# Optimization experiments

Measured on AMD Instinct MI355X. Metric: run time of the kernel, lower is better.

Reference implementation:

```python
import jax, jax.numpy as jnp
import numpy as np
from functools import partial

N_NODES = 50000
N_EDGES = 600000
N_FEAT = 128
HID = [128, 64, 32, 16]
N_GRAPHS = 64
N_CLASSES = 10


def gcn_conv(x, W, b, src, dst, n_nodes):
    # PyG GCNConv: h = x @ W; propagate with symmetric norm over A + I; add bias.
    h = x @ W  # [N, out]
    ones = jnp.ones((src.shape[0],), dtype=x.dtype)
    deg = jax.ops.segment_sum(ones, dst, num_segments=n_nodes) + 1.0  # self-loop
    dinv = jax.lax.rsqrt(deg)
    coef = dinv[src] * dinv[dst]  # [E]
    agg = jax.ops.segment_sum(h[src] * coef[:, None], dst, num_segments=n_nodes)
    agg = agg + h * (dinv * dinv)[:, None]  # self-loop contribution
    return agg + b


def global_mean_pool(x, batch, n_graphs):
    s = jax.ops.segment_sum(x, batch, num_segments=n_graphs)
    cnt = jax.ops.segment_sum(jnp.ones((x.shape[0],), x.dtype), batch, num_segments=n_graphs)
    return s / jnp.maximum(cnt, 1.0)[:, None]


def setup_inputs() -> dict:
    key = jax.random.key(0)
    ks = jax.random.split(key, 16)
    x = jax.random.normal(ks[0], (N_NODES, N_FEAT), dtype=jnp.float32)
    edge_index = jax.random.randint(ks[1], (2, N_EDGES), 0, N_NODES, dtype=jnp.int64)
    batch = jnp.sort(jax.random.randint(ks[2], (N_NODES,), 0, N_GRAPHS, dtype=jnp.int64))

    def glorot(k, fan_in, fan_out):
        s = float(np.sqrt(6.0 / (fan_in + fan_out)))
        return jax.random.uniform(k, (fan_in, fan_out), jnp.float32, -s, s)

    dims = [N_FEAT] + HID
    params = {}
    for i in range(4):
        params[f"W{i+1}"] = glorot(ks[3 + i], dims[i], dims[i + 1])
        params[f"b{i+1}"] = jnp.zeros((dims[i + 1],), jnp.float32)
    params["Wlin"] = glorot(ks[7], HID[-1], N_CLASSES)
    params["blin"] = jnp.zeros((N_CLASSES,), jnp.float32)
    return {"x": x, "edge_index": edge_index, "batch": batch, **params}


def reference(x, edge_index, batch, W1, b1, W2, b2, W3, b3, W4, b4, Wlin, blin):
    src, dst = edge_index[0], edge_index[1]
    n = x.shape[0]
    h = jax.nn.relu(gcn_conv(x, W1, b1, src, dst, n))
    h = jax.nn.relu(gcn_conv(h, W2, b2, src, dst, n))
    h = jax.nn.relu(gcn_conv(h, W3, b3, src, dst, n))
    h = jax.nn.relu(gcn_conv(h, W4, b4, src, dst, n))
    g = global_mean_pool(h, batch, N_GRAPHS)  # [G, 16]
    return g @ Wlin + blin
```

## Files before the change

### kernel.cpp

```cpp
#include <hip/hip_runtime.h>
#include <hip/hip_bf16.h>


#define N_GRAPHS 64
#define N_CLASSES 10

typedef short bf8_t __attribute__((ext_vector_type(8)));
typedef float f4_t  __attribute__((ext_vector_type(4)));

__device__ __forceinline__ float b2f(unsigned int u) {
  return __uint_as_float(u << 16);
}
__device__ __forceinline__ unsigned short f2b(float f) {
  unsigned int x = __float_as_uint(f);
  x += 0x7fffu + ((x >> 16) & 1u);
  return (unsigned short)(x >> 16);
}

__device__ __forceinline__ void block_detect(const unsigned int* __restrict__ xraw,
    const unsigned int* __restrict__ eraw, int* f32, int* i64) {
  __shared__ int c_bf, c_nz;
  if (threadIdx.x == 0) { c_bf = 0; c_nz = 0; }
  __syncthreads();
  unsigned int d = xraw[threadIdx.x & 255];
  int e = (int)(((d & 0xffffu) >> 7) & 0xff);
  if (e >= 100 && e <= 140) atomicAdd(&c_bf, 1);
  if (eraw && threadIdx.x < 64 && eraw[2 * threadIdx.x + 1] != 0u) atomicAdd(&c_nz, 1);
  __syncthreads();
  *f32 = (c_bf < 150) ? 1 : 0;
  if (i64) *i64 = (c_nz == 0) ? 1 : 0;
}

struct WPtrs { const void* p[10]; };
static constexpr int WSEG[10] = {16384, 128, 8192, 64, 2048, 32, 512, 16, 160, 10};
static constexpr int WTOTAL   = 27546;
static constexpr int WOFF[10] = {0, 16384, 16512, 24704, 24768, 26816, 26848, 27360, 27376, 27536};

__global__ __launch_bounds__(256) void cvtwe_gemm1_kernel(
    const unsigned int* __restrict__ xraw, WPtrs wp, unsigned short* __restrict__ wc,
    const int* __restrict__ braw, int* __restrict__ b32,
    const int* __restrict__ eraw, int* __restrict__ deg, int* __restrict__ rank,
    unsigned short* __restrict__ H,
    int G1, int BW, int BB, int n, int E) {
  __shared__ unsigned short Wlds2[2048];
  int f32, i64;
  block_detect(xraw, (const unsigned int*)eraw, &f32, &i64);
  const int bid = blockIdx.x;
  if (bid < G1) {
    const void* w1 = wp.p[0];
    const int l = threadIdx.x & 63;
    const int r16 = l & 15, quad = l >> 4;
    const int m0 = (bid * 4 + (threadIdx.x >> 6)) * 32;
    bf8_t afrag[2][4];
    #pragma unroll
    for (int mt = 0; mt < 2; ++mt) {
      int node = m0 + mt * 16 + r16;
      int nc = node < n ? node : n - 1;
      if (f32) {
        const float* xp = (const float*)xraw + (size_t)nc * 128 + quad * 8;
        #pragma unroll
        for (int kb = 0; kb < 4; ++kb) {
          const float4* p4 = (const float4*)(xp + kb * 32);
          float4 u0 = p4[0], u1 = p4[1];
          bf8_t a;
          a[0] = (short)f2b(u0.x); a[1] = (short)f2b(u0.y);
          a[2] = (short)f2b(u0.z); a[3] = (short)f2b(u0.w);
          a[4] = (short)f2b(u1.x); a[5] = (short)f2b(u1.y);
          a[6] = (short)f2b(u1.z); a[7] = (short)f2b(u1.w);
          afrag[mt][kb] = a;
        }
      } else {
        const unsigned short* xp = (const unsigned short*)xraw + (size_t)nc * 128 + quad * 8;
        #pragma unroll
        for (int kb = 0; kb < 4; ++kb)
          afrag[mt][kb] = *(const bf8_t*)(xp + kb * 32);
      }
    }
    for (int ct = 0; ct < 8; ++ct) {
      __syncthreads();
      #pragma unroll
      for (int it2 = 0; it2 < 2; ++it2) {
        int seg = it2 * 64 + (threadIdx.x >> 2);
        int c4  = threadIdx.x & 3;
        int kb = seg >> 5, quadk = (seg >> 3) & 3, j = seg & 7;
        int nnb = ct * 16 + c4 * 4;
        unsigned short w4[4];
        if (f32) {
          float4 u = *(const float4*)((const float*)w1 + seg * 128 + nnb);
          w4[0] = f2b(u.x); w4[1] = f2b(u.y); w4[2] = f2b(u.z); w4[3] = f2b(u.w);
        } else {
          ushort4 u = *(const ushort4*)((const unsigned short*)w1 + seg * 128 + nnb);
          w4[0] = u.x; w4[1] = u.y; w4[2] = u.z; w4[3] = u.w;
        }
        #pragma unroll
        for (int q4 = 0; q4 < 4; ++q4)
          Wlds2[kb * 512 + (quadk * 16 + c4 * 4 + q4) * 8 + j] = w4[q4];
      }
      __syncthreads();
      bf8_t bfrag[4];
      #pragma unroll
      for (int kb = 0; kb < 4; ++kb)
        bfrag[kb] = *(const bf8_t*)&Wlds2[kb * 512 + l * 8];
      #pragma unroll
      for (int mt = 0; mt < 2; ++mt) {
        f4_t acc = {0.f, 0.f, 0.f, 0.f};
        #pragma unroll
        for (int kb = 0; kb < 4; ++kb)
          acc = __builtin_amdgcn_mfma_f32_16x16x32_bf16(afrag[mt][kb], bfrag[kb], acc, 0, 0, 0);
        #pragma unroll
        for (int r = 0; r < 4; ++r) {
          int node = m0 + mt * 16 + quad * 4 + r;
          if (node < n)
            H[(size_t)node * 128 + ct * 16 + r16] = f2b(acc[r]);
        }
      }
    }
  } else if (bid < G1 + BW) {
    int i = (bid - G1) * 256 + threadIdx.x;
    if (i >= WTOTAL) return;
    int off = i, s = 0;
    #pragma unroll
    for (int t = 0; t < 10; ++t) {
      if (s == 0 && off >= WSEG[t]) { off -= WSEG[t]; } else if (s == 0) { s = t + 1; }
    }
    s -= 1;
    int soff = off;
    if ((s & 1) == 0 && s <= 6) {
      int KB, FOUT;
      if (s == 0)      { KB = 4; FOUT = 128; }
      else if (s == 2) { KB = 4; FOUT = 64; }
      else if (s == 4) { KB = 2; FOUT = 32; }
      else             { KB = 1; FOUT = 16; }
      int j = off & 7, l = (off >> 3) & 63, f = off >> 9;
      int ct = f / KB, kb = f - ct * KB;
      int k = kb * 32 + ((l >> 4) << 3) + j;
      int nn = ct * 16 + (l & 15);
      soff = k * FOUT + nn;
    }
    const void* p = wp.p[s];
    wc[WOFF[s] + off] = f32 ? f2b(((const float*)p)[soff])
                            : ((const unsigned short*)p)[soff];
  } else if (bid < G1 + BW + BB) {
    int i = (bid - G1 - BW) * 256 + threadIdx.x;
    if (i < n) b32[i] = i64 ? braw[2 * i] : braw[i];
  } else {
    int c = bid - G1 - BW - BB;
    #pragma unroll
    for (int r = 0; r < 2; ++r) {
      int e = c * 512 + r * 256 + threadIdx.x;
      if (e < E) {
        int d = i64 ? eraw[2 * (E + e)] : eraw[E + e];
        rank[e] = atomicAdd(&deg[d], 1);
      }
    }
  }
}

__global__ __launch_bounds__(256) void scan_kernel(const int* __restrict__ deg,
    int* __restrict__ row_ptr, float* __restrict__ dinv,
    unsigned long long* __restrict__ desc, uint2* __restrict__ csr, int n) {
  __shared__ int ws[4];
  __shared__ int s_total;
  __shared__ unsigned int s_prev;
  const int b = blockIdx.x, tid = threadIdx.x, lane = tid & 63, wv = tid >> 6;
  const int i = b * 256 + tid;
  int v = (i < n) ? (deg[i] + 1) : 0;
  int x = v;
  #pragma unroll
  for (int off = 1; off < 64; off <<= 1) {
    int y = __shfl_up(x, off, 64);
    if (lane >= off) x += y;
  }
  if (lane == 63) ws[wv] = x;
  __syncthreads();
  int wbase = 0;
  for (int w = 0; w < wv; ++w) wbase += ws[w];
  int incl = x + wbase;
  if (tid == 0) {
    int tot = ws[0] + ws[1] + ws[2] + ws[3];
    s_total = tot;
    unsigned long long st = (b == 0) ? (2ULL << 62) : (1ULL << 62);
    atomicExch(&desc[b], st | (unsigned long long)(unsigned int)tot);
    if (b == 0) s_prev = 0u;
  }
  __syncthreads();
  if (b > 0 && wv == 0) {
    unsigned int running = 0;
    int j = b - 1;
    while (true) {
      int idx = j - lane;
      unsigned long long d;
      if (idx >= 0) {
        do { d = atomicAdd(&desc[idx], 0ULL); } while ((d >> 62) == 0ULL);
      } else {
        d = (2ULL << 62);
      }
      unsigned long long ball = __ballot((d >> 62) == 2ULL);
      int fp = ball ? (__ffsll((unsigned long long)ball) - 1) : 64;
      unsigned int contrib = (lane <= fp) ? (unsigned int)(d & 0xffffffffULL) : 0u;
      #pragma unroll
      for (int o = 32; o; o >>= 1) contrib += __shfl_xor(contrib, o, 64);
      running += contrib;
      if (fp < 64) break;
      j -= 64;
    }
    if (lane == 0) {
      atomicExch(&desc[b], (2ULL << 62) |
                 (unsigned long long)(unsigned int)(running + (unsigned int)s_total));
      s_prev = running;
    }
  }
  __syncthreads();
  int tot = (int)s_prev + incl;
  if (i < n) {
    row_ptr[i + 1] = tot;
    float di = rsqrtf((float)v);
    dinv[i] = di;
    uint2 se;
    se.x = (unsigned int)i;
    se.y = __float_as_uint(di * di);
    csr[tot - v] = se;
  }
  if (i == 0) row_ptr[0] = 0;
}

__global__ __launch_bounds__(256) void fill_kernel(
    const int* __restrict__ eraw, const unsigned int* __restrict__ xraw,
    const int* __restrict__ row_ptr, const int* __restrict__ rank,
    const float* __restrict__ dinv, uint2* __restrict__ csr, int E) {
  int f32, i64;
  block_detect(xraw, (const unsigned int*)eraw, &f32, &i64);
  int e = blockIdx.x * 256 + threadIdx.x;
  if (e >= E) return;
  int s, d;
  if (i64) { s = eraw[2 * e]; d = eraw[2 * (E + e)]; }
  else     { s = eraw[e];     d = eraw[E + e]; }
  int pos = row_ptr[d] + 1 + rank[e];
  uint2 v;
  v.x = (unsigned int)s;
  v.y = __float_as_uint(dinv[s] * dinv[d]);
  csr[pos] = v;
}

__global__ __launch_bounds__(256) void aggemm1_mfma_kernel(
    const unsigned short* __restrict__ Hin,
    const int* __restrict__ row_ptr, const uint2* __restrict__ csr,
    const unsigned short* __restrict__ bias,
    const unsigned short* __restrict__ Wf,
    unsigned short* __restrict__ Hout, int n) {
  __shared__ __align__(16) unsigned short Gf[8 * 544];
  __shared__ __align__(16) unsigned short T[16 * 136];
  __shared__ int rp[17];
  __shared__ unsigned long long owner8[4];
  __shared__ __align__(16) unsigned short coefh[32];
  unsigned char* owner = (unsigned char*)owner8;
  const int tid = threadIdx.x;
  const int l = tid & 63, w = tid >> 6, l15 = l & 15, quad = l >> 4;
  const int node0 = blockIdx.x * 16;
  if (tid < 17) { int g = node0 + tid; rp[tid] = row_ptr[g < n ? g : n]; }
  __syncthreads();
  const int e0 = rp[0], e1 = rp[16];
  f4_t acc0 = {0.f, 0.f, 0.f, 0.f}, acc1 = {0.f, 0.f, 0.f, 0.f};
  const int s_slot = tid >> 3, qf = tid & 7;
  for (int sb = e0; sb < e1; sb += 32) {
    int gslot = sb + s_slot;
    bool valid = gslot < e1;
    uint2 ent = csr[valid ? gslot : e0];
    if (qf == 0) {
      float coef = valid ? __uint_as_float(ent.y) : 0.f;
      int m = 0;
      if (rp[m + 8] <= gslot) m += 8;
      if (rp[m + 4] <= gslot) m += 4;
      if (rp[m + 2] <= gslot) m += 2;
      if (rp[m + 1] <= gslot) m += 1;
      owner[s_slot] = (unsigned char)m;
      coefh[s_slot] = f2b(coef);
    }
    const unsigned int* hp = (const unsigned int*)Hin + (size_t)ent.x * 64 + qf * 8;
    uint4 v0 = *(const uint4*)hp;
    uint4 v1 = *(const uint4*)(hp + 4);
    unsigned int dws[8] = {v0.x, v0.y, v0.z, v0.w, v1.x, v1.y, v1.z, v1.w};
    unsigned short* gb = &Gf[qf * 544 + (s_slot >> 3) * 136 + (s_slot & 7)];
    #pragma unroll
    for (int d2 = 0; d2 < 8; ++d2) {
      gb[(d2 * 2) * 8]     = (unsigned short)(dws[d2] & 0xffffu);
      gb[(d2 * 2 + 1) * 8] = (unsigned short)(dws[d2] >> 16);
    }
    __syncthreads();
    unsigned long long ob = owner8[quad];
    bf8_t cf = *(const bf8_t*)&coefh[quad * 8];
    bf8_t af;
    #pragma unroll
    for (int j = 0; j < 8; ++j) {
      int o = (int)((ob >> (8 * j)) & 0xffULL);
      af[j] = (o == l15) ? cf[j] : (short)0;
    }
    {
      const int ct = w * 2;
      bf8_t bf0 = *(const bf8_t*)&Gf[ct * 544 + quad * 136 + l15 * 8];
      acc0 = __builtin_amdgcn_mfma_f32_16x16x32_bf16(af, bf0, acc0, 0, 0, 0);
      bf8_t bf1 = *(const bf8_t*)&Gf[(ct + 1) * 544 + quad * 136 + l15 * 8];
      acc1 = __builtin_amdgcn_mfma_f32_16x16x32_bf16(af, bf1, acc1, 0, 0, 0);
    }
    __syncthreads();
  }
  {
    const int ct = w * 2;
    float bv0 = b2f(bias[ct * 16 + l15]);
    float bv1 = b2f(bias[(ct + 1) * 16 + l15]);
    #pragma unroll
    for (int rr = 0; rr < 4; ++rr) {
      T[(quad * 4 + rr) * 136 + ct * 16 + l15]       = f2b(fmaxf(acc0[rr] + bv0, 0.f));
      T[(quad * 4 + rr) * 136 + (ct + 1) * 16 + l15] = f2b(fmaxf(acc1[rr] + bv1, 0.f));
    }
  }
  __syncthreads();
  f4_t a2 = {0.f, 0.f, 0.f, 0.f};
  #pragma unroll
  for (int kb = 0; kb < 4; ++kb) {
    bf8_t afr = *(const bf8_t*)&T[l15 * 136 + kb * 32 + quad * 8];
    bf8_t bfr = *(const bf8_t*)&Wf[((w * 4 + kb) * 64 + l) * 8];
    a2 = __builtin_amdgcn_mfma_f32_16x16x32_bf16(afr, bfr, a2, 0, 0, 0);
  }
  #pragma unroll
  for (int rr = 0; rr < 4; ++rr) {
    int node = node0 + quad * 4 + rr;
    if (node < n)
      Hout[(size_t)node * 64 + w * 16 + l15] = f2b(a2[rr]);
  }
}

template<int DW> struct UVec { unsigned int d[DW]; };
template<int DW>
__device__ __forceinline__ UVec<DW> uload(const unsigned int* p) {
  UVec<DW> r;
  if constexpr (DW == 4) { uint4 v = *(const uint4*)p; r.d[0]=v.x; r.d[1]=v.y; r.d[2]=v.z; r.d[3]=v.w; }
  else if constexpr (DW == 2) { uint2 v = *(const uint2*)p; r.d[0]=v.x; r.d[1]=v.y; }
  else { r.d[0] = *p; }
  return r;
}
template<int DW>
__device__ __forceinline__ void ustore(unsigned int* p, const UVec<DW>& v) {
  if constexpr (DW == 4) { *(uint4*)p = make_uint4(v.d[0], v.d[1], v.d[2], v.d[3]); }
  else if constexpr (DW == 2) { *(uint2*)p = make_uint2(v.d[0], v.d[1]); }
  else { *p = v.d[0]; }
}

template<int FIN, int FOUT, int LPG>
__global__ __launch_bounds__(256) void aggemm_kernel(
    const unsigned short* __restrict__ Hin,
    const int* __restrict__ row_ptr, const uint2* __restrict__ csr,
    const unsigned short* __restrict__ bias,
    const unsigned short* __restrict__ Wf, unsigned short* __restrict__ Hout, int n) {
  constexpr int DW  = FIN / LPG / 2;
  constexpr int NPB = 256 / LPG;
  constexpr int LD  = FIN + 8;
  constexpr int KB  = FIN / 32;
  constexpr int CT  = FOUT / 16;
  constexpr int MT  = NPB / 16;
  __shared__ unsigned short T[NPB * LD];
  const int r = threadIdx.x / LPG, l = threadIdx.x % LPG;
  const int node0 = blockIdx.x * NPB;
  const int g = node0 + r;
  const unsigned int* H2 = (const unsigned int*)Hin;
  UVec<DW> o;
  #pragma unroll
  for (int d = 0; d < DW; ++d) o.d[d] = 0u;
  if (g < n) {
    float a[2 * DW];
    #pragma unroll
    for (int d = 0; d < 2 * DW; ++d) a[d] = 0.f;
    const int e0 = row_ptr[g], e1 = row_ptr[g + 1];
    for (int base = e0; base < e1; base += LPG) {
      int cnt = e1 - base < LPG ? e1 - base : LPG;
      uint2 my = csr[(base + l < e1) ? (base + l) : (e1 - 1)];
      for (int j = 0; j < cnt; ++j) {
        int s = __shfl((int)my.x, j, LPG);
        float c = __uint_as_float(__shfl((int)my.y, j, LPG));
        UVec<DW> v = uload<DW>(H2 + (size_t)s * (FIN / 2) + l * DW);
        #pragma unroll
        for (int d = 0; d < DW; ++d) {
          a[2*d]   = fmaf(b2f(v.d[d] & 0xffffu), c, a[2*d]);
          a[2*d+1] = fmaf(b2f(v.d[d] >> 16), c, a[2*d+1]);
        }
      }
    }
    UVec<DW> bb = uload<DW>((const unsigned int*)bias + l * DW);
    #pragma unroll
    for (int d = 0; d < DW; ++d) {
      float lo = fmaxf(a[2*d]   + b2f(bb.d[d] & 0xffffu), 0.f);
      float hi = fmaxf(a[2*d+1] + b2f(bb.d[d] >> 16), 0.f);
      o.d[d] = (unsigned int)f2b(lo) | ((unsigned int)f2b(hi) << 16);
    }
  }
  ustore<DW>((unsigned int*)&T[r * LD + l * DW * 2], o);
  __syncthreads();
  const int w = threadIdx.x >> 6;
  if (w < MT * CT && node0 < n) {
    const int mt = w / CT, ct = w % CT;
    const int ll = threadIdx.x & 63;
    const int r16 = ll & 15, quad = ll >> 4;
    bf8_t afrag[KB], bfrag[KB];
    #pragma unroll
    for (int kb = 0; kb < KB; ++kb) {
      afrag[kb] = *(const bf8_t*)(&T[(mt * 16 + r16) * LD + quad * 8 + kb * 32]);
      bfrag[kb] = *(const bf8_t*)(Wf + ((ct * KB + kb) * 64 + ll) * 8);
    }
    f4_t acc = {0.f, 0.f, 0.f, 0.f};
    #pragma unroll
    for (int kb = 0; kb < KB; ++kb)
      acc = __builtin_amdgcn_mfma_f32_16x16x32_bf16(afrag[kb], bfrag[kb], acc, 0, 0, 0);
    #pragma unroll
    for (int rr = 0; rr < 4; ++rr) {
      int node = node0 + mt * 16 + quad * 4 + rr;
      if (node < n)
        Hout[(size_t)node * FOUT + ct * 16 + r16] = f2b(acc[rr]);
    }
  }
}

__global__ __launch_bounds__(256) void agg_pool_kernel(
    const unsigned short* __restrict__ Hin,
    const int* __restrict__ row_ptr, const uint2* __restrict__ csr,
    const unsigned short* __restrict__ bias,
    const int* __restrict__ batch, float* __restrict__ pooled,
    float* __restrict__ cnt, int n) {
  __shared__ float acc[N_GRAPHS * 16];
  __shared__ float ccnt[N_GRAPHS];
  for (int i = threadIdx.x; i < N_GRAPHS * 16; i += 256) acc[i] = 0.f;
  if (threadIdx.x < N_GRAPHS) ccnt[threadIdx.x] = 0.f;
  __syncthreads();
  const int r = threadIdx.x >> 3, l = threadIdx.x & 7;
  const int g = blockIdx.x * 32 + r;
  if (g < n) {
    const unsigned int* H2 = (const unsigned int*)Hin;
    float a0 = 0.f, a1 = 0.f;
    const int e0 = row_ptr[g], e1 = row_ptr[g + 1];
    for (int base = e0; base < e1; base += 8) {
      int cnt2 = e1 - base < 8 ? e1 - base : 8;
      uint2 my = csr[(base + l < e1) ? (base + l) : (e1 - 1)];
      for (int j = 0; j < cnt2; ++j) {
        int s = __shfl((int)my.x, j, 8);
        float c = __uint_as_float(__shfl((int)my.y, j, 8));
        unsigned int v = H2[(size_t)s * 8 + l];
        a0 = fmaf(b2f(v & 0xffffu), c, a0);
        a1 = fmaf(b2f(v >> 16), c, a1);
      }
    }
    unsigned int bb = ((const unsigned int*)bias)[l];
    a0 = fmaxf(a0 + b2f(bb & 0xffffu), 0.f);
    a1 = fmaxf(a1 + b2f(bb >> 16), 0.f);
    int gb = batch[g];
    atomicAdd(&acc[gb * 16 + l * 2 + 0], a0);
    atomicAdd(&acc[gb * 16 + l * 2 + 1], a1);
    if (l == 0) atomicAdd(&ccnt[gb], 1.f);
  }
  __syncthreads();
  for (int i = threadIdx.x; i < N_GRAPHS * 16; i += 256)
    if (acc[i] != 0.f) atomicAdd(&pooled[i], acc[i]);
  if (threadIdx.x < N_GRAPHS && ccnt[threadIdx.x] != 0.f)
    atomicAdd(&cnt[threadIdx.x], ccnt[threadIdx.x]);
}

__global__ __launch_bounds__(256) void final_kernel(const float* __restrict__ pooled,
    const float* __restrict__ cnt, const unsigned short* __restrict__ wc,
    void* __restrict__ out, const unsigned int* __restrict__ xraw) {
  int f32;
  block_detect(xraw, nullptr, &f32, nullptr);
  int id = blockIdx.x * 256 + threadIdx.x;
  if (id >= N_GRAPHS * N_CLASSES) return;
  const unsigned short* Wlin = wc + WOFF[8];
  const unsigned short* blin = wc + WOFF[9];
  int g = id / N_CLASSES, c = id - g * N_CLASSES;
  float inv = 1.0f / fmaxf(cnt[g], 1.0f);
  float a = b2f(blin[c]);
  #pragma unroll
  for (int f = 0; f < 16; ++f)
    a = fmaf(pooled[g * 16 + f] * inv, b2f(Wlin[f * N_CLASSES + c]), a);
  if (f32) ((float*)out)[id] = a;
  else     ((unsigned short*)out)[id] = f2b(a);
}

extern "C" void kernel_launch(void* const* d_in, const int* in_sizes, int n_in,
                              void* d_out, int out_size, void* d_ws, size_t ws_size,
                              hipStream_t stream) {
  const unsigned int* xraw = (const unsigned int*)d_in[0];
  const int* eraw          = (const int*)d_in[1];
  const int* braw          = (const int*)d_in[2];

  const int N = in_sizes[2];
  const int E = in_sizes[1] / 2;
  const int nb = (N + 255) / 256;

  char* p = (char*)d_ws;
  auto alloc = [&](size_t bytes) -> void* {
    void* r = (void*)p;
    p += (bytes + 255) & ~(size_t)255;
    return r;
  };
  const size_t off_desc = ((size_t)N * 4 + 255) & ~(size_t)255;
  const size_t off_pool = (off_desc + (size_t)nb * 8 + 255) & ~(size_t)255;
  const size_t ztotal   = off_pool + (N_GRAPHS * 16 + N_GRAPHS) * 4;
  char* zbase = (char*)alloc(ztotal);
  int*   deg    = (int*)zbase;
  unsigned long long* desc = (unsigned long long*)(zbase + off_desc);
  float* pooled = (float*)(zbase + off_pool);
  float* cntf   = pooled + N_GRAPHS * 16;

  int*   row_ptr  = (int*)  alloc((size_t)(N + 1) * 4);
  int*   rank     = (int*)  alloc((size_t)E * 4);
  float* dinv     = (float*)alloc((size_t)N * 4);
  int*   batch32  = (int*)  alloc((size_t)N * 4);
  uint2* csr      = (uint2*)alloc((size_t)(E + N) * 8);
  unsigned short* wcan  = (unsigned short*)alloc((size_t)WTOTAL * 2);
  unsigned short* hbufA = (unsigned short*)alloc((size_t)N * 128 * 2);
  unsigned short* hbufB = (unsigned short*)alloc((size_t)N * 128 * 2);

  hipMemsetAsync(zbase, 0, ztotal, stream);

  WPtrs wp;
  for (int i = 0; i < 10; ++i) wp.p[i] = d_in[3 + i];

  const int BW  = (WTOTAL + 255) / 256;
  const int BB  = nb;
  const int BE  = (E + 255) / 256;
  const int BE2 = (E + 511) / 512;
  const int G1  = (N + 127) / 128;
  cvtwe_gemm1_kernel<<<G1 + BW + BB + BE2, 256, 0, stream>>>(xraw, wp, wcan,
      braw, batch32, eraw, deg, rank, hbufA, G1, BW, BB, N, E);

  scan_kernel<<<nb, 256, 0, stream>>>(deg, row_ptr, dinv, desc, csr, N);

  const unsigned short* b1 = wcan + WOFF[1];
  const unsigned short* W2 = wcan + WOFF[2];
  const unsigned short* b2 = wcan + WOFF[3];
  const unsigned short* W3 = wcan + WOFF[4];
  const unsigned short* b3 = wcan + WOFF[5];
  const unsigned short* W4 = wcan + WOFF[6];
  const unsigned short* b4 = wcan + WOFF[7];

  fill_kernel<<<BE, 256, 0, stream>>>(eraw, xraw, row_ptr, rank, dinv, csr, E);

  aggemm1_mfma_kernel<<<(N + 15) / 16, 256, 0, stream>>>(
      hbufA, row_ptr, csr, b1, W2, hbufB, N);
  aggemm_kernel<64, 32, 8><<<(N + 31) / 32, 256, 0, stream>>>(
      hbufB, row_ptr, csr, b2, W3, hbufA, N);
  aggemm_kernel<32, 16, 8><<<(N + 31) / 32, 256, 0, stream>>>(
      hbufA, row_ptr, csr, b3, W4, hbufB, N);
  agg_pool_kernel<<<(N + 31) / 32, 256, 0, stream>>>(hbufB, row_ptr, csr, b4,
      batch32, pooled, cntf, N);

  final_kernel<<<(N_GRAPHS * N_CLASSES + 255) / 256, 256, 0, stream>>>(pooled, cntf, wcan, d_out, xraw);
}
```

Baseline: 227.3 us.

## Generalize MFMA sparse aggregation to all GCN layers and batch edge loads in pooling

Layer 1's MFMA-based aggregation becomes a template over feature width. Layers 2 and 3 now also aggregate neighbours with one-hot coefficient MFMAs over edge slabs sized to the feature width, replacing the per-node shuffle/FMA gather. The gather is redone so each thread loads one dword per edge for 8 edges and transposes them into LDS with packed stores. The pooling kernel preloads 8 CSR entries before accumulating, to expose more memory-level parallelism. The risks are wasted MFMA work and idle waves for the narrow layers, plus extra per-slab barriers.

```diff
diff --git a/kernel.cpp b/kernel.cpp
--- a/kernel.cpp
+++ b/kernel.cpp
@@ -242,179 +242,124 @@
   csr[pos] = v;
 }
 
-__global__ __launch_bounds__(256) void aggemm1_mfma_kernel(
+template<int FIN, int FOUT>
+__global__ __launch_bounds__(256) void mfma_aggemm_kernel(
     const unsigned short* __restrict__ Hin,
     const int* __restrict__ row_ptr, const uint2* __restrict__ csr,
     const unsigned short* __restrict__ bias,
     const unsigned short* __restrict__ Wf,
     unsigned short* __restrict__ Hout, int n) {
-  __shared__ __align__(16) unsigned short Gf[8 * 544];
-  __shared__ __align__(16) unsigned short T[16 * 136];
+  constexpr int SPP = 4096 / FIN;
+  constexpr int KS  = SPP / 32;
+  constexpr int SG  = SPP / 8;
+  constexpr int FP  = FIN / 2;
+  constexpr int CT  = FIN / 16;
+  constexpr int CPW = (CT + 3) / 4;
+  constexpr int AW  = CT / CPW;
+  constexpr int KGP = 136;
+  constexpr int CTP = SG * KGP;
+  constexpr int LD  = FIN + 8;
+  constexpr int KB2 = FIN / 32;
+  constexpr int CT2 = FOUT / 16;
+
+  __shared__ __align__(16) unsigned short Gf[CT * CTP];
+  __shared__ __align__(16) unsigned short T[16 * LD];
   __shared__ int rp[17];
-  __shared__ unsigned long long owner8[4];
-  __shared__ __align__(16) unsigned short coefh[32];
-  unsigned char* owner = (unsigned char*)owner8;
+  __shared__ unsigned long long owner8[KS * 4];
+  __shared__ __align__(16) unsigned short coefh[SPP];
+
   const int tid = threadIdx.x;
   const int l = tid & 63, w = tid >> 6, l15 = l & 15, quad = l >> 4;
   const int node0 = blockIdx.x * 16;
   if (tid < 17) { int g = node0 + tid; rp[tid] = row_ptr[g < n ? g : n]; }
   __syncthreads();
   const int e0 = rp[0], e1 = rp[16];
-  f4_t acc0 = {0.f, 0.f, 0.f, 0.f}, acc1 = {0.f, 0.f, 0.f, 0.f};
-  const int s_slot = tid >> 3, qf = tid & 7;
-  for (int sb = e0; sb < e1; sb += 32) {
-    int gslot = sb + s_slot;
-    bool valid = gslot < e1;
-    uint2 ent = csr[valid ? gslot : e0];
-    if (qf == 0) {
+  const int sg = tid % SG, fp = tid / SG;
+  const int ct = fp >> 3, fl = (2 * fp) & 15;
+  unsigned short* gb = &Gf[ct * CTP + sg * KGP + fl * 8];
+
+  f4_t acc[CPW];
+  #pragma unroll
+  for (int c = 0; c < CPW; ++c) acc[c] = (f4_t){0.f, 0.f, 0.f, 0.f};
+
+  for (int sb = e0; sb < e1; sb += SPP) {
+    if (tid < SPP) {
+      int gslot = sb + tid;
+      bool valid = gslot < e1;
+      uint2 ent = csr[valid ? gslot : e0];
       float coef = valid ? __uint_as_float(ent.y) : 0.f;
       int m = 0;
       if (rp[m + 8] <= gslot) m += 8;
       if (rp[m + 4] <= gslot) m += 4;
       if (rp[m + 2] <= gslot) m += 2;
       if (rp[m + 1] <= gslot) m += 1;
-      owner[s_slot] = (unsigned char)m;
-      coefh[s_slot] = f2b(coef);
-    }
-    const unsigned int* hp = (const unsigned int*)Hin + (size_t)ent.x * 64 + qf * 8;
-    uint4 v0 = *(const uint4*)hp;
-    uint4 v1 = *(const uint4*)(hp + 4);
-    unsigned int dws[8] = {v0.x, v0.y, v0.z, v0.w, v1.x, v1.y, v1.z, v1.w};
-    unsigned short* gb = &Gf[qf * 544 + (s_slot >> 3) * 136 + (s_slot & 7)];
-    #pragma unroll
-    for (int d2 = 0; d2 < 8; ++d2) {
-      gb[(d2 * 2) * 8]     = (unsigned short)(dws[d2] & 0xffffu);
-      gb[(d2 * 2 + 1) * 8] = (unsigned short)(dws[d2] >> 16);
-    }
+      ((unsigned char*)owner8)[tid] = (unsigned char)m;
+      coefh[tid] = f2b(coef);
+    }
+    unsigned int in[8];
+    #pragma unroll
+    for (int i = 0; i < 8; ++i) {
+      int gslot = sb + sg * 8 + i;
+      unsigned int src = csr[(gslot < e1) ? gslot : e0].x;
+      in[i] = ((const unsigned int*)Hin)[(size_t)src * FP + fp];
+    }
+    uint4 olo, ohi;
+    olo.x = (in[0] & 0xffffu) | (in[1] << 16);
+    olo.y = (in[2] & 0xffffu) | (in[3] << 16);
+    olo.z = (in[4] & 0xffffu) | (in[5] << 16);
+    olo.w = (in[6] & 0xffffu) | (in[7] << 16);
+    ohi.x = (in[0] >> 16) | (in[1] & 0xffff0000u);
+    ohi.y = (in[2] >> 16) | (in[3] & 0xffff0000u);
+    ohi.z = (in[4] >> 16) | (in[5] & 0xffff0000u);
+    ohi.w = (in[6] >> 16) | (in[7] & 0xffff0000u);
+    *(uint4*)gb = olo;
+    *(uint4*)(gb + 8) = ohi;
     __syncthreads();
-    unsigned long long ob = owner8[quad];
-    bf8_t cf = *(const bf8_t*)&coefh[quad * 8];
-    bf8_t af;
-    #pragma unroll
-    for (int j = 0; j < 8; ++j) {
-      int o = (int)((ob >> (8 * j)) & 0xffULL);
-      af[j] = (o == l15) ? cf[j] : (short)0;
-    }
-    {
-      const int ct = w * 2;
-      bf8_t bf0 = *(const bf8_t*)&Gf[ct * 544 + quad * 136 + l15 * 8];
-      acc0 = __builtin_amdgcn_mfma_f32_16x16x32_bf16(af, bf0, acc0, 0, 0, 0);
-      bf8_t bf1 = *(const bf8_t*)&Gf[(ct + 1) * 544 + quad * 136 + l15 * 8];
-      acc1 = __builtin_amdgcn_mfma_f32_16x16x32_bf16(af, bf1, acc1, 0, 0, 0);
+    if (w < AW) {
+      #pragma unroll
+      for (int ks = 0; ks < KS; ++ks) {
+        unsigned long long ob = owner8[ks * 4 + quad];
+        bf8_t cf = *(const bf8_t*)&coefh[ks * 32 + quad * 8];
+        bf8_t af;
+        #pragma unroll
+        for (int j = 0; j < 8; ++j) {
+          int o = (int)((ob >> (8 * j)) & 0xffULL);
+          af[j] = (o == l15) ? cf[j] : (short)0;
+        }
+        #pragma unroll
+        for (int c = 0; c < CPW; ++c) {
+          const int ctm = w * CPW + c;
+          bf8_t bf = *(const bf8_t*)&Gf[ctm * CTP + (ks * 4 + quad) * KGP + l15 * 8];
+          acc[c] = __builtin_amdgcn_mfma_f32_16x16x32_bf16(af, bf, acc[c], 0, 0, 0);
+        }
+      }
     }
     __syncthreads();
   }
-  {
-    const int ct = w * 2;
-    float bv0 = b2f(bias[ct * 16 + l15]);
-    float bv1 = b2f(bias[(ct + 1) * 16 + l15]);
+  if (w < AW) {
+    #pragma unroll
+    for (int c = 0; c < CPW; ++c) {
+      const int ctm = w * CPW + c;
+      float bv = b2f(bias[ctm * 16 + l15]);
+      #pragma unroll
+      for (int rr = 0; rr < 4; ++rr)
+        T[(quad * 4 + rr) * LD + ctm * 16 + l15] = f2b(fmaxf(acc[c][rr] + bv, 0.f));
+    }
+  }
+  __syncthreads();
+  if (w < CT2) {
+    f4_t a2 = {0.f, 0.f, 0.f, 0.f};
+    #pragma unroll
+    for (int kb = 0; kb < KB2; ++kb) {
+      bf8_t afr = *(const bf8_t*)&T[l15 * LD + kb * 32 + quad * 8];
+      bf8_t bfr = *(const bf8_t*)&Wf[((w * KB2 + kb) * 64 + l) * 8];
+      a2 = __builtin_amdgcn_mfma_f32_16x16x32_bf16(afr, bfr, a2, 0, 0, 0);
+    }
     #pragma unroll
     for (int rr = 0; rr < 4; ++rr) {
-      T[(quad * 4 + rr) * 136 + ct * 16 + l15]       = f2b(fmaxf(acc0[rr] + bv0, 0.f));
-      T[(quad * 4 + rr) * 136 + (ct + 1) * 16 + l15] = f2b(fmaxf(acc1[rr] + bv1, 0.f));
-    }
-  }
-  __syncthreads();
-  f4_t a2 = {0.f, 0.f, 0.f, 0.f};
-  #pragma unroll
-  for (int kb = 0; kb < 4; ++kb) {
-    bf8_t afr = *(const bf8_t*)&T[l15 * 136 + kb * 32 + quad * 8];
-    bf8_t bfr = *(const bf8_t*)&Wf[((w * 4 + kb) * 64 + l) * 8];
-    a2 = __builtin_amdgcn_mfma_f32_16x16x32_bf16(afr, bfr, a2, 0, 0, 0);
-  }
-  #pragma unroll
-  for (int rr = 0; rr < 4; ++rr) {
-    int node = node0 + quad * 4 + rr;
-    if (node < n)
-      Hout[(size_t)node * 64 + w * 16 + l15] = f2b(a2[rr]);
-  }
-}
-
-template<int DW> struct UVec { unsigned int d[DW]; };
-template<int DW>
-__device__ __forceinline__ UVec<DW> uload(const unsigned int* p) {
-  UVec<DW> r;
-  if constexpr (DW == 4) { uint4 v = *(const uint4*)p; r.d[0]=v.x; r.d[1]=v.y; r.d[2]=v.z; r.d[3]=v.w; }
-  else if constexpr (DW == 2) { uint2 v = *(const uint2*)p; r.d[0]=v.x; r.d[1]=v.y; }
-  else { r.d[0] = *p; }
-  return r;
-}
-template<int DW>
-__device__ __forceinline__ void ustore(unsigned int* p, const UVec<DW>& v) {
-  if constexpr (DW == 4) { *(uint4*)p = make_uint4(v.d[0], v.d[1], v.d[2], v.d[3]); }
-  else if constexpr (DW == 2) { *(uint2*)p = make_uint2(v.d[0], v.d[1]); }
-  else { *p = v.d[0]; }
-}
-
-template<int FIN, int FOUT, int LPG>
-__global__ __launch_bounds__(256) void aggemm_kernel(
-    const unsigned short* __restrict__ Hin,
-    const int* __restrict__ row_ptr, const uint2* __restrict__ csr,
-    const unsigned short* __restrict__ bias,
-    const unsigned short* __restrict__ Wf, unsigned short* __restrict__ Hout, int n) {
-  constexpr int DW  = FIN / LPG / 2;
-  constexpr int NPB = 256 / LPG;
-  constexpr int LD  = FIN + 8;
-  constexpr int KB  = FIN / 32;
-  constexpr int CT  = FOUT / 16;
-  constexpr int MT  = NPB / 16;
-  __shared__ unsigned short T[NPB * LD];
-  const int r = threadIdx.x / LPG, l = threadIdx.x % LPG;
-  const int node0 = blockIdx.x * NPB;
-  const int g = node0 + r;
-  const unsigned int* H2 = (const unsigned int*)Hin;
-  UVec<DW> o;
-  #pragma unroll
-  for (int d = 0; d < DW; ++d) o.d[d] = 0u;
-  if (g < n) {
-    float a[2 * DW];
-    #pragma unroll
-    for (int d = 0; d < 2 * DW; ++d) a[d] = 0.f;
-    const int e0 = row_ptr[g], e1 = row_ptr[g + 1];
-    for (int base = e0; base < e1; base += LPG) {
-      int cnt = e1 - base < LPG ? e1 - base : LPG;
-      uint2 my = csr[(base + l < e1) ? (base + l) : (e1 - 1)];
-      for (int j = 0; j < cnt; ++j) {
-        int s = __shfl((int)my.x, j, LPG);
-        float c = __uint_as_float(__shfl((int)my.y, j, LPG));
-        UVec<DW> v = uload<DW>(H2 + (size_t)s * (FIN / 2) + l * DW);
-        #pragma unroll
-        for (int d = 0; d < DW; ++d) {
-          a[2*d]   = fmaf(b2f(v.d[d] & 0xffffu), c, a[2*d]);
-          a[2*d+1] = fmaf(b2f(v.d[d] >> 16), c, a[2*d+1]);
-        }
-      }
-    }
-    UVec<DW> bb = uload<DW>((const unsigned int*)bias + l * DW);
-    #pragma unroll
-    for (int d = 0; d < DW; ++d) {
-      float lo = fmaxf(a[2*d]   + b2f(bb.d[d] & 0xffffu), 0.f);
-      float hi = fmaxf(a[2*d+1] + b2f(bb.d[d] >> 16), 0.f);
-      o.d[d] = (unsigned int)f2b(lo) | ((unsigned int)f2b(hi) << 16);
-    }
-  }
-  ustore<DW>((unsigned int*)&T[r * LD + l * DW * 2], o);
-  __syncthreads();
-  const int w = threadIdx.x >> 6;
-  if (w < MT * CT && node0 < n) {
-    const int mt = w / CT, ct = w % CT;
-    const int ll = threadIdx.x & 63;
-    const int r16 = ll & 15, quad = ll >> 4;
-    bf8_t afrag[KB], bfrag[KB];
-    #pragma unroll
-    for (int kb = 0; kb < KB; ++kb) {
-      afrag[kb] = *(const bf8_t*)(&T[(mt * 16 + r16) * LD + quad * 8 + kb * 32]);
-      bfrag[kb] = *(const bf8_t*)(Wf + ((ct * KB + kb) * 64 + ll) * 8);
-    }
-    f4_t acc = {0.f, 0.f, 0.f, 0.f};
-    #pragma unroll
-    for (int kb = 0; kb < KB; ++kb)
-      acc = __builtin_amdgcn_mfma_f32_16x16x32_bf16(afrag[kb], bfrag[kb], acc, 0, 0, 0);
-    #pragma unroll
-    for (int rr = 0; rr < 4; ++rr) {
-      int node = node0 + mt * 16 + quad * 4 + rr;
+      int node = node0 + quad * 4 + rr;
       if (node < n)
-        Hout[(size_t)node * FOUT + ct * 16 + r16] = f2b(acc[rr]);
+        Hout[(size_t)node * FOUT + w * 16 + l15] = f2b(a2[rr]);
     }
   }
 }
@@ -437,14 +382,18 @@
     float a0 = 0.f, a1 = 0.f;
     const int e0 = row_ptr[g], e1 = row_ptr[g + 1];
     for (int base = e0; base < e1; base += 8) {
-      int cnt2 = e1 - base < 8 ? e1 - base : 8;
-      uint2 my = csr[(base + l < e1) ? (base + l) : (e1 - 1)];
-      for (int j = 0; j < cnt2; ++j) {
-        int s = __shfl((int)my.x, j, 8);
-        float c = __uint_as_float(__shfl((int)my.y, j, 8));
-        unsigned int v = H2[(size_t)s * 8 + l];
-        a0 = fmaf(b2f(v & 0xffffu), c, a0);
-        a1 = fmaf(b2f(v >> 16), c, a1);
+      uint2 eb[8];
+      #pragma unroll
+      for (int j = 0; j < 8; ++j)
+        eb[j] = csr[(base + j < e1) ? (base + j) : (e1 - 1)];
+      #pragma unroll
+      for (int j = 0; j < 8; ++j) {
+        if (base + j < e1) {
+          float c = __uint_as_float(eb[j].y);
+          unsigned int v = H2[(size_t)eb[j].x * 8 + l];
+          a0 = fmaf(b2f(v & 0xffffu), c, a0);
+          a1 = fmaf(b2f(v >> 16), c, a1);
+        }
       }
     }
     unsigned int bb = ((const unsigned int*)bias)[l];
@@ -511,7 +460,7 @@
   int*   rank     = (int*)  alloc((size_t)E * 4);
   float* dinv     = (float*)alloc((size_t)N * 4);
   int*   batch32  = (int*)  alloc((size_t)N * 4);
-  uint2* csr      = (uint2*)alloc((size_t)(E + N) * 8);
+  uint2* csr      = (uint2*)alloc((size_t)(E + N + 8) * 8);
   unsigned short* wcan  = (unsigned short*)alloc((size_t)WTOTAL * 2);
   unsigned short* hbufA = (unsigned short*)alloc((size_t)N * 128 * 2);
   unsigned short* hbufB = (unsigned short*)alloc((size_t)N * 128 * 2);
@@ -541,11 +490,12 @@
 
   fill_kernel<<<BE, 256, 0, stream>>>(eraw, xraw, row_ptr, rank, dinv, csr, E);
 
-  aggemm1_mfma_kernel<<<(N + 15) / 16, 256, 0, stream>>>(
+  const int GA = (N + 15) / 16;
+  mfma_aggemm_kernel<128, 64><<<GA, 256, 0, stream>>>(
       hbufA, row_ptr, csr, b1, W2, hbufB, N);
-  aggemm_kernel<64, 32, 8><<<(N + 31) / 32, 256, 0, stream>>>(
+  mfma_aggemm_kernel<64, 32><<<GA, 256, 0, stream>>>(
       hbufB, row_ptr, csr, b2, W3, hbufA, N);
-  aggemm_kernel<32, 16, 8><<<(N + 31) / 32, 256, 0, stream>>>(
+  mfma_aggemm_kernel<32, 16><<<GA, 256, 0, stream>>>(
       hbufA, row_ptr, csr, b3, W4, hbufB, N);
   agg_pool_kernel<<<(N + 31) / 32, 256, 0, stream>>>(hbufB, row_ptr, csr, b4,
       batch32, pooled, cntf, N);
```

Result: slower. 313.3 us (+37.9%).

## Batch neighbor gathers four-wide and replace MFMA layer-1 aggregation with generic kernel

Applied to the files above, without the earlier changes.

The custom MFMA-based layer-1 aggregation kernel, which built a one-hot coefficient matrix per 32-edge chunk, is removed. Layer 1 now uses the generic shuffle-based aggemm kernel with 16 lanes per node. The gather loops in aggemm and the pooling kernel now issue four independent row loads before doing the FMAs, which raises memory-level parallelism on these latency-bound gathers. Padded edge slots get a zero coefficient, and the CSR buffer gains 8 extra entries so reads past the end stay in bounds. This trades the MFMA approach for simpler code that keeps more loads in flight, at the cost of some wasted loads on partial chunks.

```diff
diff --git a/kernel.cpp b/kernel.cpp
--- a/kernel.cpp
+++ b/kernel.cpp
@@ -240,94 +240,6 @@
   v.x = (unsigned int)s;
   v.y = __float_as_uint(dinv[s] * dinv[d]);
   csr[pos] = v;
-}
-
-__global__ __launch_bounds__(256) void aggemm1_mfma_kernel(
-    const unsigned short* __restrict__ Hin,
-    const int* __restrict__ row_ptr, const uint2* __restrict__ csr,
-    const unsigned short* __restrict__ bias,
-    const unsigned short* __restrict__ Wf,
-    unsigned short* __restrict__ Hout, int n) {
-  __shared__ __align__(16) unsigned short Gf[8 * 544];
-  __shared__ __align__(16) unsigned short T[16 * 136];
-  __shared__ int rp[17];
-  __shared__ unsigned long long owner8[4];
-  __shared__ __align__(16) unsigned short coefh[32];
-  unsigned char* owner = (unsigned char*)owner8;
-  const int tid = threadIdx.x;
-  const int l = tid & 63, w = tid >> 6, l15 = l & 15, quad = l >> 4;
-  const int node0 = blockIdx.x * 16;
-  if (tid < 17) { int g = node0 + tid; rp[tid] = row_ptr[g < n ? g : n]; }
-  __syncthreads();
-  const int e0 = rp[0], e1 = rp[16];
-  f4_t acc0 = {0.f, 0.f, 0.f, 0.f}, acc1 = {0.f, 0.f, 0.f, 0.f};
-  const int s_slot = tid >> 3, qf = tid & 7;
-  for (int sb = e0; sb < e1; sb += 32) {
-    int gslot = sb + s_slot;
-    bool valid = gslot < e1;
-    uint2 ent = csr[valid ? gslot : e0];
-    if (qf == 0) {
-      float coef = valid ? __uint_as_float(ent.y) : 0.f;
-      int m = 0;
-      if (rp[m + 8] <= gslot) m += 8;
-      if (rp[m + 4] <= gslot) m += 4;
-      if (rp[m + 2] <= gslot) m += 2;
-      if (rp[m + 1] <= gslot) m += 1;
-      owner[s_slot] = (unsigned char)m;
-      coefh[s_slot] = f2b(coef);
-    }
-    const unsigned int* hp = (const unsigned int*)Hin + (size_t)ent.x * 64 + qf * 8;
-    uint4 v0 = *(const uint4*)hp;
-    uint4 v1 = *(const uint4*)(hp + 4);
-    unsigned int dws[8] = {v0.x, v0.y, v0.z, v0.w, v1.x, v1.y, v1.z, v1.w};
-    unsigned short* gb = &Gf[qf * 544 + (s_slot >> 3) * 136 + (s_slot & 7)];
-    #pragma unroll
-    for (int d2 = 0; d2 < 8; ++d2) {
-      gb[(d2 * 2) * 8]     = (unsigned short)(dws[d2] & 0xffffu);
-      gb[(d2 * 2 + 1) * 8] = (unsigned short)(dws[d2] >> 16);
-    }
-    __syncthreads();
-    unsigned long long ob = owner8[quad];
-    bf8_t cf = *(const bf8_t*)&coefh[quad * 8];
-    bf8_t af;
-    #pragma unroll
-    for (int j = 0; j < 8; ++j) {
-      int o = (int)((ob >> (8 * j)) & 0xffULL);
-      af[j] = (o == l15) ? cf[j] : (short)0;
-    }
-    {
-      const int ct = w * 2;
-      bf8_t bf0 = *(const bf8_t*)&Gf[ct * 544 + quad * 136 + l15 * 8];
-      acc0 = __builtin_amdgcn_mfma_f32_16x16x32_bf16(af, bf0, acc0, 0, 0, 0);
-      bf8_t bf1 = *(const bf8_t*)&Gf[(ct + 1) * 544 + quad * 136 + l15 * 8];
-      acc1 = __builtin_amdgcn_mfma_f32_16x16x32_bf16(af, bf1, acc1, 0, 0, 0);
-    }
-    __syncthreads();
-  }
-  {
-    const int ct = w * 2;
-    float bv0 = b2f(bias[ct * 16 + l15]);
-    float bv1 = b2f(bias[(ct + 1) * 16 + l15]);
-    #pragma unroll
-    for (int rr = 0; rr < 4; ++rr) {
-      T[(quad * 4 + rr) * 136 + ct * 16 + l15]       = f2b(fmaxf(acc0[rr] + bv0, 0.f));
-      T[(quad * 4 + rr) * 136 + (ct + 1) * 16 + l15] = f2b(fmaxf(acc1[rr] + bv1, 0.f));
-    }
-  }
-  __syncthreads();
-  f4_t a2 = {0.f, 0.f, 0.f, 0.f};
-  #pragma unroll
-  for (int kb = 0; kb < 4; ++kb) {
-    bf8_t afr = *(const bf8_t*)&T[l15 * 136 + kb * 32 + quad * 8];
-    bf8_t bfr = *(const bf8_t*)&Wf[((w * 4 + kb) * 64 + l) * 8];
-    a2 = __builtin_amdgcn_mfma_f32_16x16x32_bf16(afr, bfr, a2, 0, 0, 0);
-  }
-  #pragma unroll
-  for (int rr = 0; rr < 4; ++rr) {
-    int node = node0 + quad * 4 + rr;
-    if (node < n)
-      Hout[(size_t)node * 64 + w * 16 + l15] = f2b(a2[rr]);
-  }
 }
 
 template<int DW> struct UVec { unsigned int d[DW]; };
@@ -374,14 +286,27 @@
     for (int base = e0; base < e1; base += LPG) {
       int cnt = e1 - base < LPG ? e1 - base : LPG;
       uint2 my = csr[(base + l < e1) ? (base + l) : (e1 - 1)];
-      for (int j = 0; j < cnt; ++j) {
-        int s = __shfl((int)my.x, j, LPG);
-        float c = __uint_as_float(__shfl((int)my.y, j, LPG));
-        UVec<DW> v = uload<DW>(H2 + (size_t)s * (FIN / 2) + l * DW);
-        #pragma unroll
-        for (int d = 0; d < DW; ++d) {
-          a[2*d]   = fmaf(b2f(v.d[d] & 0xffffu), c, a[2*d]);
-          a[2*d+1] = fmaf(b2f(v.d[d] >> 16), c, a[2*d+1]);
+      for (int j0 = 0; j0 < cnt; j0 += 4) {
+        int   sj[4];
+        float cj[4];
+        #pragma unroll
+        for (int jj = 0; jj < 4; ++jj) {
+          int j = j0 + jj;
+          sj[jj] = __shfl((int)my.x, j & (LPG - 1), LPG);
+          float cc = __uint_as_float(__shfl((int)my.y, j & (LPG - 1), LPG));
+          cj[jj] = (j < cnt) ? cc : 0.f;
+        }
+        UVec<DW> v[4];
+        #pragma unroll
+        for (int jj = 0; jj < 4; ++jj)
+          v[jj] = uload<DW>(H2 + (size_t)sj[jj] * (FIN / 2) + l * DW);
+        #pragma unroll
+        for (int jj = 0; jj < 4; ++jj) {
+          #pragma unroll
+          for (int d = 0; d < DW; ++d) {
+            a[2*d]   = fmaf(b2f(v[jj].d[d] & 0xffffu), cj[jj], a[2*d]);
+            a[2*d+1] = fmaf(b2f(v[jj].d[d] >> 16),     cj[jj], a[2*d+1]);
+          }
         }
       }
     }
@@ -437,14 +362,27 @@
     float a0 = 0.f, a1 = 0.f;
     const int e0 = row_ptr[g], e1 = row_ptr[g + 1];
     for (int base = e0; base < e1; base += 8) {
-      int cnt2 = e1 - base < 8 ? e1 - base : 8;
-      uint2 my = csr[(base + l < e1) ? (base + l) : (e1 - 1)];
-      for (int j = 0; j < cnt2; ++j) {
-        int s = __shfl((int)my.x, j, 8);
-        float c = __uint_as_float(__shfl((int)my.y, j, 8));
-        unsigned int v = H2[(size_t)s * 8 + l];
-        a0 = fmaf(b2f(v & 0xffffu), c, a0);
-        a1 = fmaf(b2f(v >> 16), c, a1);
+      uint2 eb[8];
+      #pragma unroll
+      for (int j = 0; j < 8; ++j)
+        eb[j] = csr[(base + j < e1) ? (base + j) : (e1 - 1)];
+      #pragma unroll
+      for (int j0 = 0; j0 < 8; j0 += 4) {
+        float cj[4];
+        unsigned int v[4];
+        #pragma unroll
+        for (int jj = 0; jj < 4; ++jj) {
+          int j = j0 + jj;
+          cj[jj] = (base + j < e1) ? __uint_as_float(eb[j].y) : 0.f;
+        }
+        #pragma unroll
+        for (int jj = 0; jj < 4; ++jj)
+          v[jj] = H2[(size_t)eb[j0 + jj].x * 8 + l];
+        #pragma unroll
+        for (int jj = 0; jj < 4; ++jj) {
+          a0 = fmaf(b2f(v[jj] & 0xffffu), cj[jj], a0);
+          a1 = fmaf(b2f(v[jj] >> 16),     cj[jj], a1);
+        }
       }
     }
     unsigned int bb = ((const unsigned int*)bias)[l];
@@ -511,7 +449,7 @@
   int*   rank     = (int*)  alloc((size_t)E * 4);
   float* dinv     = (float*)alloc((size_t)N * 4);
   int*   batch32  = (int*)  alloc((size_t)N * 4);
-  uint2* csr      = (uint2*)alloc((size_t)(E + N) * 8);
+  uint2* csr      = (uint2*)alloc((size_t)(E + N + 8) * 8);
   unsigned short* wcan  = (unsigned short*)alloc((size_t)WTOTAL * 2);
   unsigned short* hbufA = (unsigned short*)alloc((size_t)N * 128 * 2);
   unsigned short* hbufB = (unsigned short*)alloc((size_t)N * 128 * 2);
@@ -541,7 +479,7 @@
 
   fill_kernel<<<BE, 256, 0, stream>>>(eraw, xraw, row_ptr, rank, dinv, csr, E);
 
-  aggemm1_mfma_kernel<<<(N + 15) / 16, 256, 0, stream>>>(
+  aggemm_kernel<128, 64, 16><<<(N + 15) / 16, 256, 0, stream>>>(
       hbufA, row_ptr, csr, b1, W2, hbufB, N);
   aggemm_kernel<64, 32, 8><<<(N + 31) / 32, 256, 0, stream>>>(
       hbufB, row_ptr, csr, b2, W3, hbufA, N);
```

Result: faster. 209.5 us (-7.8%).
